# Performance work log

Measured on AMD Instinct MI355X. Metric: run time of the kernel, lower is better.

Reference implementation:

```python
import jax, jax.numpy as jnp
import numpy as np

KERNEL_MUL = 2.0
KERNEL_NUM = 5


def _mmd(source, target, kernel_mul=KERNEL_MUL, kernel_num=KERNEL_NUM, fix_sigma=None):
    n = source.shape[0]
    total = jnp.concatenate([source, target], axis=0)  # [2N, D]
    n_samples = total.shape[0]
    # Pairwise squared L2 distances via Gram matrix (same math as the
    # broadcasted (2N,2N,D) diff-square-sum, but O(N^2 D) GEMM instead).
    sq = jnp.sum(total * total, axis=1)                # [2N]
    gram = total @ total.T                             # [2N, 2N]
    L2 = sq[:, None] + sq[None, :] - 2.0 * gram        # [2N, 2N]
    if fix_sigma:
        bandwidth = fix_sigma
    else:
        # torch used L2_distance.data -> detached; match with stop_gradient
        bandwidth = jax.lax.stop_gradient(jnp.sum(L2)) / (n_samples ** 2 - n_samples)
    bandwidth = bandwidth / (kernel_mul ** (kernel_num // 2))
    kernels = jnp.zeros_like(L2)
    for i in range(kernel_num):
        kernels = kernels + jnp.exp(-L2 / (bandwidth * kernel_mul ** i))
    XX = kernels[:n, :n]
    YY = kernels[n:, n:]
    XY = kernels[:n, n:]
    YX = kernels[n:, :n]
    return jnp.mean(XX + YY - XY - YX)


def setup_inputs() -> dict:
    key = jax.random.key(0)
    k1, k2 = jax.random.split(key)
    N, D = 4096, 512
    source = jax.random.normal(k1, (N, D), dtype=jnp.float32)
    target = jax.random.normal(k2, (N, D), dtype=jnp.float32)
    return {"source": source, "target": target}


def reference(source, target):
    # MMD_sample_size = inf >= batch_size -> single full-batch MMD
    return _mmd(source, target)
```

## Files before the change

### kernel.cpp

```cpp
#include <hip/hip_runtime.h>
#include <hip/hip_fp16.h>


#define NS 8192
#define D_DIM 512
#define NTILE 64
#define NBLK 2080

typedef _Float16 f16x8 __attribute__((ext_vector_type(8)));
typedef float f32x4 __attribute__((ext_vector_type(4)));

__global__ __launch_bounds__(256) void prep(const float* __restrict__ src,
                                            const float* __restrict__ tgt,
                                            __half* __restrict__ Th,
                                            float* __restrict__ sq,
                                            float* __restrict__ colsum,
                                            float* __restrict__ Sacc) {
    __shared__ float lcs[4][D_DIM];
    __shared__ float wsq[4];
    int tid = threadIdx.x, w = tid >> 6, l = tid & 63;
    int r0 = blockIdx.x * 16 + w * 4;
    float cs[8];
#pragma unroll
    for (int j = 0; j < 8; ++j) cs[j] = 0.f;
    float ws = 0.f;

#pragma unroll
    for (int rr = 0; rr < 4; ++rr) {
        int r = r0 + rr;
        const float* rowp = (r < 4096) ? (src + (size_t)r * D_DIM)
                                       : (tgt + (size_t)(r - 4096) * D_DIM);
        float4 v0 = *reinterpret_cast<const float4*>(rowp + l * 8);
        float4 v1 = *reinterpret_cast<const float4*>(rowp + l * 8 + 4);
        float f[8] = {v0.x, v0.y, v0.z, v0.w, v1.x, v1.y, v1.z, v1.w};
        __half h[8];
        float s = 0.f;
#pragma unroll
        for (int j = 0; j < 8; ++j) {
            h[j] = __float2half(f[j]);
            float fj = __half2float(h[j]);
            s += fj * fj;
            cs[j] += fj;
        }
        *reinterpret_cast<int4*>(Th + (size_t)r * D_DIM + l * 8) =
            *reinterpret_cast<const int4*>(h);
#pragma unroll
        for (int off = 32; off; off >>= 1) s += __shfl_xor(s, off, 64);
        if (l == 0) { sq[r] = s; ws += s; }
    }
    if (l == 0) wsq[w] = ws;
#pragma unroll
    for (int j = 0; j < 8; ++j) lcs[w][l * 8 + j] = cs[j];
    __syncthreads();
#pragma unroll
    for (int j = 0; j < 2; ++j) {
        int c = tid * 2 + j;
        float v = (lcs[0][c] + lcs[1][c]) + (lcs[2][c] + lcs[3][c]);
        atomicAdd(&colsum[c], v);
    }
    if (tid == 0) atomicAdd(Sacc, (wsq[0] + wsq[1]) + (wsq[2] + wsq[3]));
}

__global__ void compute_bw(const float* __restrict__ colsum, const float* __restrict__ Sacc,
                           float* __restrict__ cs) {
    __shared__ float red[256];
    int t = threadIdx.x;
    float c = 0.f;
    for (int i = t; i < D_DIM; i += 256) { float v = colsum[i]; c += v * v; }
    red[t] = c; __syncthreads();
    for (int off = 128; off; off >>= 1) { if (t < off) red[t] += red[t + off]; __syncthreads(); }
    if (t == 0) {
        double C = red[0];
        double S = (double)Sacc[0];
        double sumL2 = 2.0 * (double)NS * S - 2.0 * C;
        double bw = sumL2 / ((double)NS * NS - (double)NS) / 4.0;
        cs[0] = (float)(-1.4426950408889634 / bw);
    }
}

__global__ __launch_bounds__(256, 2) void mmd_main(const __half* __restrict__ Th,
                                                   const float* __restrict__ sq,
                                                   const float* __restrict__ cs,
                                                   float* __restrict__ partials) {
    __shared__ __half Ah[2][128 * 64];
    __shared__ __half Bh[2][128 * 64];
    __shared__ float wred[4];

    int borig = blockIdx.x;
    int b = (borig & 7) * (NBLK / 8) + (borig >> 3);
    int ti = 0, rem = b;
    while (rem >= NTILE - ti) { rem -= NTILE - ti; ++ti; }
    int tj = ti + rem;
    int ibase = ti * 128, jbase = tj * 128;
    float wgt = ((ti == tj) ? 1.f : 2.f) * (((ti < 32) == (tj < 32)) ? 1.f : -1.f);

    int tid = threadIdx.x;
    int wid = tid >> 6, lane = tid & 63;
    int wm = wid >> 1, wn = wid & 1;
    int cl = lane >> 4;

    f32x4 acc[4][4];
#pragma unroll
    for (int m = 0; m < 4; ++m)
#pragma unroll
        for (int n = 0; n < 4; ++n) acc[m][n] = f32x4{0.f, 0.f, 0.f, 0.f};

    auto STAGE = [&](int buf, int k0) {
#pragma unroll
        for (int it = 0; it < 4; ++it) {
            int h16 = tid + it * 256;
            int row = h16 >> 3, ch = h16 & 7;
            int scol = ((ch ^ (row & 7)) * 8);
            __builtin_amdgcn_global_load_lds(
                (const __attribute__((address_space(1))) unsigned int*)(Th + (size_t)(ibase + row) * D_DIM + k0 + scol),
                (__attribute__((address_space(3))) unsigned int*)(&Ah[buf][h16 * 8]), 16, 0, 0);
            __builtin_amdgcn_global_load_lds(
                (const __attribute__((address_space(1))) unsigned int*)(Th + (size_t)(jbase + row) * D_DIM + k0 + scol),
                (__attribute__((address_space(3))) unsigned int*)(&Bh[buf][h16 * 8]), 16, 0, 0);
        }
    };

    auto COMPUTE = [&](int buf) {
#pragma unroll
        for (int ks = 0; ks < 2; ++ks) {
            f16x8 afr[4], bfr[4];
#pragma unroll
            for (int m = 0; m < 4; ++m) {
                int ra = wm * 64 + m * 16 + (lane & 15);
                int pc = (ks * 4 + cl) ^ (ra & 7);
                afr[m] = *reinterpret_cast<const f16x8*>(&Ah[buf][ra * 64 + pc * 8]);
            }
#pragma unroll
            for (int n = 0; n < 4; ++n) {
                int rb = wn * 64 + n * 16 + (lane & 15);
                int pc = (ks * 4 + cl) ^ (rb & 7);
                bfr[n] = *reinterpret_cast<const f16x8*>(&Bh[buf][rb * 64 + pc * 8]);
            }
#pragma unroll
            for (int m = 0; m < 4; ++m)
#pragma unroll
                for (int n = 0; n < 4; ++n)
                    acc[m][n] = __builtin_amdgcn_mfma_f32_16x16x32_f16(afr[m], bfr[n], acc[m][n], 0, 0, 0);
        }
    };

    STAGE(0, 0);
    __syncthreads();
    int buf = 0;
#pragma unroll
    for (int t = 0; t < 7; ++t) {
        STAGE(buf ^ 1, (t + 1) * 64);
        COMPUTE(buf);
        __syncthreads();
        buf ^= 1;
    }
    COMPUTE(buf);

    float c0 = cs[0];
    float m2c0 = -2.f * c0;
    float sci[16], scj[4];
#pragma unroll
    for (int m = 0; m < 4; ++m)
#pragma unroll
        for (int r = 0; r < 4; ++r)
            sci[m * 4 + r] = sq[ibase + wm * 64 + m * 16 + (lane >> 4) * 4 + r] * c0;
#pragma unroll
    for (int n = 0; n < 4; ++n)
        scj[n] = sq[jbase + wn * 64 + n * 16 + (lane & 15)] * c0;

    float a0 = 0.f, a1 = 0.f, a2 = 0.f, a3 = 0.f, a4 = 0.f;
#pragma unroll
    for (int m = 0; m < 4; ++m)
#pragma unroll
        for (int n = 0; n < 4; ++n)
#pragma unroll
            for (int r = 0; r < 4; ++r) {
                float x0 = fmaf(acc[m][n][r], m2c0, sci[m * 4 + r] + scj[n]);
                float e0 = __builtin_amdgcn_exp2f(x0);
                float e1 = __builtin_amdgcn_sqrtf(e0);
                float e2 = __builtin_amdgcn_sqrtf(e1);
                float e3 = __builtin_amdgcn_sqrtf(e2);
                float e4 = __builtin_amdgcn_sqrtf(e3);
                a0 += e0; a1 += e1; a2 += e2; a3 += e3; a4 += e4;
            }
    float ksum = ((a0 + a1) + (a2 + a3)) + a4;
#pragma unroll
    for (int off = 32; off; off >>= 1) ksum += __shfl_xor(ksum, off, 64);
    if (lane == 0) wred[wid] = ksum;
    __syncthreads();
    if (tid == 0)
        partials[borig] = ((wred[0] + wred[1]) + (wred[2] + wred[3])) * wgt;
}

__global__ void finalize(const float* __restrict__ partials, float* __restrict__ out) {
    __shared__ double red[256];
    int t = threadIdx.x;
    double s = 0.0;
    for (int i = t; i < NBLK; i += 256) s += (double)partials[i];
    red[t] = s; __syncthreads();
    for (int off = 128; off; off >>= 1) { if (t < off) red[t] += red[t + off]; __syncthreads(); }
    if (t == 0) out[0] = (float)(red[0] * (1.0 / (4096.0 * 4096.0)));
}

extern "C" void kernel_launch(void* const* d_in, const int* in_sizes, int n_in,
                              void* d_out, int out_size, void* d_ws, size_t ws_size,
                              hipStream_t stream) {
    (void)in_sizes; (void)n_in; (void)out_size; (void)ws_size;
    const float* src = (const float*)d_in[0];
    const float* tgt = (const float*)d_in[1];
    char* ws = (char*)d_ws;
    __half* Th      = (__half*)ws;
    float* sq       = (float*)(ws + 8388608);
    float* colsum   = (float*)(ws + 8421376);
    float* Sacc     = (float*)(ws + 8423424);
    float* cs       = (float*)(ws + 8423428);
    float* partials = (float*)(ws + 8423432);
    float* out      = (float*)d_out;

    hipMemsetAsync(colsum, 0, 2052, stream);
    hipLaunchKernelGGL(prep, dim3(512), dim3(256), 0, stream, src, tgt, Th, sq, colsum, Sacc);
    hipLaunchKernelGGL(compute_bw, dim3(1), dim3(256), 0, stream, colsum, Sacc, cs);
    hipLaunchKernelGGL(mmd_main, dim3(NBLK), dim3(256), 0, stream, Th, sq, cs, partials);
    hipLaunchKernelGGL(finalize, dim3(1), dim3(256), 0, stream, partials, out);
}
```

Before: 161.1 us.

## Fuse bandwidth and final reduction into main kernel, relax pipeline barriers

Removes the single-block compute_bw and finalize kernels. Each main block now recomputes the bandwidth from colsum and Sacc itself, and the last-finishing block, found with an atomic counter, writes the result from a double atomic accumulator. The K-loop swaps __syncthreads for explicit vmcnt waits plus raw barriers, so the next stage's loads can stay in flight while the current buffer is consumed. This saves two launches and serial tiny kernels, at the cost of redundant per-block bandwidth math and 2080 atomics on one address.

After: 184.1 us. +14.3%, slower.

```diff
diff --git a/kernel.cpp b/kernel.cpp
--- a/kernel.cpp
+++ b/kernel.cpp
@@ -61,27 +61,13 @@
     if (tid == 0) atomicAdd(Sacc, (wsq[0] + wsq[1]) + (wsq[2] + wsq[3]));
 }
 
-__global__ void compute_bw(const float* __restrict__ colsum, const float* __restrict__ Sacc,
-                           float* __restrict__ cs) {
-    __shared__ float red[256];
-    int t = threadIdx.x;
-    float c = 0.f;
-    for (int i = t; i < D_DIM; i += 256) { float v = colsum[i]; c += v * v; }
-    red[t] = c; __syncthreads();
-    for (int off = 128; off; off >>= 1) { if (t < off) red[t] += red[t + off]; __syncthreads(); }
-    if (t == 0) {
-        double C = red[0];
-        double S = (double)Sacc[0];
-        double sumL2 = 2.0 * (double)NS * S - 2.0 * C;
-        double bw = sumL2 / ((double)NS * NS - (double)NS) / 4.0;
-        cs[0] = (float)(-1.4426950408889634 / bw);
-    }
-}
-
 __global__ __launch_bounds__(256, 2) void mmd_main(const __half* __restrict__ Th,
                                                    const float* __restrict__ sq,
-                                                   const float* __restrict__ cs,
-                                                   float* __restrict__ partials) {
+                                                   const float* __restrict__ colsum,
+                                                   const float* __restrict__ Sacc,
+                                                   unsigned int* __restrict__ cnt,
+                                                   double* __restrict__ accd,
+                                                   float* __restrict__ out) {
     __shared__ __half Ah[2][128 * 64];
     __shared__ __half Bh[2][128 * 64];
     __shared__ float wred[4];
@@ -145,19 +131,31 @@
     };
 
     STAGE(0, 0);
-    __syncthreads();
-    int buf = 0;
 #pragma unroll
     for (int t = 0; t < 7; ++t) {
-        STAGE(buf ^ 1, (t + 1) * 64);
-        COMPUTE(buf);
-        __syncthreads();
-        buf ^= 1;
-    }
-    COMPUTE(buf);
-
-    float c0 = cs[0];
+        STAGE((t + 1) & 1, (t + 1) * 64);
+        asm volatile("s_waitcnt vmcnt(8)" ::: "memory");
+        __builtin_amdgcn_s_barrier();
+        COMPUTE(t & 1);
+        asm volatile("" ::: "memory");
+        __builtin_amdgcn_s_barrier();
+    }
+    asm volatile("s_waitcnt vmcnt(0)" ::: "memory");
+    __builtin_amdgcn_s_barrier();
+    COMPUTE(7 & 1);
+
+    float4 ca = *reinterpret_cast<const float4*>(colsum + lane * 8);
+    float4 cb = *reinterpret_cast<const float4*>(colsum + lane * 8 + 4);
+    float cpart = ca.x * ca.x + ca.y * ca.y + ca.z * ca.z + ca.w * ca.w
+                + cb.x * cb.x + cb.y * cb.y + cb.z * cb.z + cb.w * cb.w;
+#pragma unroll
+    for (int off = 32; off; off >>= 1) cpart += __shfl_xor(cpart, off, 64);
+    double S = (double)Sacc[0];
+    double sumL2 = 2.0 * (double)NS * S - 2.0 * (double)cpart;
+    double bw = sumL2 / ((double)NS * NS - (double)NS) / 4.0;
+    float c0 = (float)(-1.4426950408889634 / bw);
     float m2c0 = -2.f * c0;
+
     float sci[16], scj[4];
 #pragma unroll
     for (int m = 0; m < 4; ++m)
@@ -188,18 +186,16 @@
     for (int off = 32; off; off >>= 1) ksum += __shfl_xor(ksum, off, 64);
     if (lane == 0) wred[wid] = ksum;
     __syncthreads();
-    if (tid == 0)
-        partials[borig] = ((wred[0] + wred[1]) + (wred[2] + wred[3])) * wgt;
-}
-
-__global__ void finalize(const float* __restrict__ partials, float* __restrict__ out) {
-    __shared__ double red[256];
-    int t = threadIdx.x;
-    double s = 0.0;
-    for (int i = t; i < NBLK; i += 256) s += (double)partials[i];
-    red[t] = s; __syncthreads();
-    for (int off = 128; off; off >>= 1) { if (t < off) red[t] += red[t + off]; __syncthreads(); }
-    if (t == 0) out[0] = (float)(red[0] * (1.0 / (4096.0 * 4096.0)));
+    if (tid == 0) {
+        float tot = ((wred[0] + wred[1]) + (wred[2] + wred[3])) * wgt;
+        atomicAdd(accd, (double)tot);
+        __threadfence();
+        unsigned int old = atomicAdd(cnt, 1u);
+        if (old == NBLK - 1) {
+            double total = atomicAdd(accd, 0.0);
+            out[0] = (float)(total * (1.0 / (4096.0 * 4096.0)));
+        }
+    }
 }
 
 extern "C" void kernel_launch(void* const* d_in, const int* in_sizes, int n_in,
@@ -213,13 +209,11 @@
     float* sq       = (float*)(ws + 8388608);
     float* colsum   = (float*)(ws + 8421376);
     float* Sacc     = (float*)(ws + 8423424);
-    float* cs       = (float*)(ws + 8423428);
-    float* partials = (float*)(ws + 8423432);
+    unsigned int* cnt = (unsigned int*)(ws + 8423428);
+    double* accd    = (double*)(ws + 8423432);
     float* out      = (float*)d_out;
 
-    hipMemsetAsync(colsum, 0, 2052, stream);
+    hipMemsetAsync(colsum, 0, 2064, stream);
     hipLaunchKernelGGL(prep, dim3(512), dim3(256), 0, stream, src, tgt, Th, sq, colsum, Sacc);
-    hipLaunchKernelGGL(compute_bw, dim3(1), dim3(256), 0, stream, colsum, Sacc, cs);
-    hipLaunchKernelGGL(mmd_main, dim3(NBLK), dim3(256), 0, stream, Th, sq, cs, partials);
-    hipLaunchKernelGGL(finalize, dim3(1), dim3(256), 0, stream, partials, out);
+    hipLaunchKernelGGL(mmd_main, dim3(NBLK), dim3(256), 0, stream, Th, sq, colsum, Sacc, cnt, accd, out);
 }
```
